# Kernel tuning notes

Measured on AMD Instinct MI355X. Metric: run time of the kernel, lower is better.

## Reference

```python
import jax, jax.numpy as jnp
import numpy as np

N_D, E_D = 50000, 200000
N_A, E_A = 50000, 200000
B, L, VOCAB = 256, 1000, 26


def _gat(x, src, dst, W, a_src, a_dst, bias, heads, dout, n,
         edge_attr=None, W_e=None, a_e=None):
    """PyG GATConv (eval mode: dropout off). Adds self-loops (default), edge-attr
    self-loops filled with mean (fill_value='mean' default), LeakyReLU(0.2),
    per-destination softmax, sum-aggregate, concat heads, add bias."""
    loop = jnp.arange(n, dtype=src.dtype)
    src = jnp.concatenate([src, loop])
    dst = jnp.concatenate([dst, loop])
    h = (x @ W).reshape(n, heads, dout)                      # [N,H,D]
    alpha = (h * a_src[None]).sum(-1)[src] + (h * a_dst[None]).sum(-1)[dst]  # [E',H]
    if edge_attr is not None:
        mean_e = jnp.mean(edge_attr, axis=0, keepdims=True)
        ea = jnp.concatenate([edge_attr, jnp.broadcast_to(mean_e, (n, edge_attr.shape[1]))], 0)
        he = (ea @ W_e).reshape(-1, heads, dout)             # [E',H,D]
        alpha = alpha + (he * a_e[None]).sum(-1)
    alpha = jax.nn.leaky_relu(alpha, 0.2)
    amax = jax.ops.segment_max(alpha, dst, num_segments=n)
    ex = jnp.exp(alpha - amax[dst])
    denom = jax.ops.segment_sum(ex, dst, num_segments=n)
    w = ex / (denom[dst] + 1e-16)                            # edge softmax weights
    out = jax.ops.segment_sum(h[src] * w[..., None], dst, num_segments=n)
    return out.reshape(n, heads * dout) + bias


def _conv1d(x, w):
    return jax.lax.conv_general_dilated(x, w, (1,), 'VALID',
                                        dimension_numbers=('NCH', 'OIH', 'NCH'))


def setup_inputs():
    key = jax.random.key(0)
    ks = iter(jax.random.split(key, 64))
    def nrm(shape, s=0.1):
        return jax.random.normal(next(ks), shape, jnp.float32) * s
    inp = {}
    inp['drug_x'] = nrm((N_D, 78), 1.0)
    inp['drug_edge_index'] = jax.random.randint(next(ks), (2, E_D), 0, N_D, jnp.int32)
    inp['drug_batch'] = ((jnp.arange(N_D) * B) // N_D).astype(jnp.int32)
    inp['target_tokens'] = jax.random.randint(next(ks), (B, L), 0, VOCAB, jnp.int32)
    inp['a2h_x'] = nrm((N_A, 24), 1.0)
    inp['a2h_edge_index'] = jax.random.randint(next(ks), (2, E_A), 0, N_A, jnp.int32)
    inp['a2h_edge_attr'] = nrm((E_A, 5), 1.0)
    inp['a2h_batch'] = ((jnp.arange(N_A) * B) // N_A).astype(jnp.int32)
    inp['gat1_w'] = nrm((78, 390)); inp['gat1_att_src'] = nrm((5, 78)); inp['gat1_att_dst'] = nrm((5, 78)); inp['gat1_bias'] = jnp.zeros((390,), jnp.float32)
    inp['gat2_w'] = nrm((390, 128)); inp['gat2_att_src'] = nrm((1, 128)); inp['gat2_att_dst'] = nrm((1, 128)); inp['gat2_bias'] = jnp.zeros((128,), jnp.float32)
    inp['fc_g1_w'] = nrm((128, 128)); inp['fc_g1_b'] = jnp.zeros((128,), jnp.float32)
    inp['embed_xt'] = nrm((VOCAB, 128), 1.0)
    inp['conv1_w'] = nrm((64, 128, 5)); inp['conv1_b'] = jnp.zeros((64,), jnp.float32)
    inp['conv2_w'] = nrm((32, 64, 3)); inp['conv2_b'] = jnp.zeros((32,), jnp.float32)
    inp['fc_xt1_w'] = nrm((32, 128)); inp['fc_xt1_b'] = jnp.zeros((128,), jnp.float32)
    inp['ag1_w'] = nrm((24, 320)); inp['ag1_att_src'] = nrm((5, 64)); inp['ag1_att_dst'] = nrm((5, 64)); inp['ag1_lin_edge'] = nrm((5, 320)); inp['ag1_att_edge'] = nrm((5, 64)); inp['ag1_bias'] = jnp.zeros((320,), jnp.float32)
    inp['ag2_w'] = nrm((320, 128)); inp['ag2_att_src'] = nrm((1, 128)); inp['ag2_att_dst'] = nrm((1, 128)); inp['ag2_lin_edge'] = nrm((5, 128)); inp['ag2_att_edge'] = nrm((1, 128)); inp['ag2_bias'] = jnp.zeros((128,), jnp.float32)
    inp['a2h_fc1_w'] = nrm((128, 128)); inp['a2h_fc1_b'] = jnp.zeros((128,), jnp.float32)
    inp['fc1_w'] = nrm((384, 1024)); inp['fc1_b'] = jnp.zeros((1024,), jnp.float32)
    inp['fc2_w'] = nrm((1024, 256)); inp['fc2_b'] = jnp.zeros((256,), jnp.float32)
    inp['out_w'] = nrm((256, 1)); inp['out_b'] = jnp.zeros((1,), jnp.float32)
    return inp


def reference(drug_x, drug_edge_index, drug_batch, target_tokens,
              a2h_x, a2h_edge_index, a2h_edge_attr, a2h_batch,
              gat1_w, gat1_att_src, gat1_att_dst, gat1_bias,
              gat2_w, gat2_att_src, gat2_att_dst, gat2_bias,
              fc_g1_w, fc_g1_b, embed_xt,
              conv1_w, conv1_b, conv2_w, conv2_b, fc_xt1_w, fc_xt1_b,
              ag1_w, ag1_att_src, ag1_att_dst, ag1_lin_edge, ag1_att_edge, ag1_bias,
              ag2_w, ag2_att_src, ag2_att_dst, ag2_lin_edge, ag2_att_edge, ag2_bias,
              a2h_fc1_w, a2h_fc1_b, fc1_w, fc1_b, fc2_w, fc2_b, out_w, out_b):
    # drug GAT branch (dropout is identity in eval mode)
    x = jax.nn.elu(_gat(drug_x, drug_edge_index[0], drug_edge_index[1],
                        gat1_w, gat1_att_src, gat1_att_dst, gat1_bias, 5, 78, N_D))
    x = jax.nn.relu(_gat(x, drug_edge_index[0], drug_edge_index[1],
                         gat2_w, gat2_att_src, gat2_att_dst, gat2_bias, 1, 128, N_D))
    x = jax.ops.segment_max(x, drug_batch, num_segments=B)        # global_max_pool
    x = jax.nn.relu(x @ fc_g1_w + fc_g1_b)
    # protein CNN branch
    e = embed_xt[target_tokens]                                   # [B,L,128]
    c = jnp.transpose(e, (0, 2, 1))                               # [B,128,L]
    c = jax.nn.relu(_conv1d(c, conv1_w) + conv1_b[None, :, None])
    c = jax.nn.relu(_conv1d(c, conv2_w) + conv2_b[None, :, None])
    xt = jnp.max(c, axis=-1) @ fc_xt1_w + fc_xt1_b                # AdaptiveMaxPool1d(1)
    # a2h GAT branch with edge features
    a = jax.nn.elu(_gat(a2h_x, a2h_edge_index[0], a2h_edge_index[1],
                        ag1_w, ag1_att_src, ag1_att_dst, ag1_bias, 5, 64, N_A,
                        a2h_edge_attr, ag1_lin_edge, ag1_att_edge))
    a = jax.nn.relu(_gat(a, a2h_edge_index[0], a2h_edge_index[1],
                         ag2_w, ag2_att_src, ag2_att_dst, ag2_bias, 1, 128, N_A,
                         a2h_edge_attr, ag2_lin_edge, ag2_att_edge))
    a = jax.ops.segment_max(a, a2h_batch, num_segments=B)
    a = jax.nn.relu(a @ a2h_fc1_w + a2h_fc1_b)
    # fusion head
    xc = jnp.concatenate([x, xt, a], axis=1)                      # [B,384]
    xc = jax.nn.relu(xc @ fc1_w + fc1_b)
    xc = jax.nn.relu(xc @ fc2_w + fc2_b)
    return xc @ out_w + out_b                                     # [B,1]
```

## Files before the change

kernel.cpp:

```cpp
#include <hip/hip_runtime.h>

#define NN 50000
#define EE 200000
#define BB 256
#define LL 1000

static inline int cdiv(int a, int b){ return (a + b - 1) / b; }

typedef __attribute__((ext_vector_type(4))) float f32x4;
typedef __attribute__((ext_vector_type(2))) float f32x2;
typedef __attribute__((ext_vector_type(8))) short bf16x8;

__device__ inline short f2bf(float f){
  unsigned u = __float_as_uint(f);
  unsigned r = u + 0x7fffu + ((u >> 16) & 1u);
  return (short)(r >> 16);
}
__device__ inline float bf2f(short s){
  return __uint_as_float(((unsigned)(unsigned short)s) << 16);
}

__global__ void zero_kernel(unsigned* __restrict__ p, long n){
  long i = (long)blockIdx.x*blockDim.x + threadIdx.x;
  long st = (long)gridDim.x*blockDim.x;
  for(; i < n; i += st) p[i] = 0u;
}

__global__ __launch_bounds__(256) void gemm_splitk_kernel(
    const float* __restrict__ A, const float* __restrict__ B,
    float* __restrict__ part, int M, int N, int K, int KS){
  __shared__ float As[32][17];
  const int tid = threadIdx.x;
  const int col = blockIdx.x*64 + (tid & 63);
  const int rg = tid >> 6;
  const int row0 = blockIdx.y*32;
  const int kc = (K + KS - 1) / KS;
  const int k0 = blockIdx.z * kc;
  const int k1 = min(k0 + kc, K);
  float acc[8] = {};
  for(int kb = k0; kb < k1; kb += 16){
    int kn = min(16, k1 - kb);
    for(int i = tid; i < 32*16; i += 256){
      int r = i >> 4, kk = i & 15;
      int gr = row0 + r;
      As[r][kk] = (gr < M && kb + kk < k1) ? A[(long)gr*K + kb + kk] : 0.f;
    }
    __syncthreads();
    if(col < N){
      for(int kk = 0; kk < kn; kk++){
        float b = B[(long)(kb+kk)*N + col];
        #pragma unroll
        for(int i = 0; i < 8; i++)
          acc[i] = fmaf(As[rg*8 + i][kk], b, acc[i]);
      }
    }
    __syncthreads();
  }
  if(col < N){
    #pragma unroll
    for(int i = 0; i < 8; i++){
      int r = row0 + rg*8 + i;
      if(r < M) part[((long)blockIdx.z*M + r)*N + col] = acc[i];
    }
  }
}

template<int ACT>
__global__ void splitk_reduce_kernel(const float* __restrict__ part,
                                     const float* __restrict__ bias,
                                     float* __restrict__ C,
                                     int M, int N, int KS, int ldc){
  int idx = blockIdx.x*256 + threadIdx.x;
  if(idx >= M*N) return;
  int r = idx / N, c = idx - r*N;
  float s = 0.f;
  for(int z = 0; z < KS; z++) s += part[((long)z*M + r)*N + c];
  s += bias[c];
  if(ACT == 1) s = fmaxf(s, 0.f);
  C[(long)r*ldc + c] = s;
}

__global__ __launch_bounds__(256) void gemm_mfma_bf16_kernel(
    const float* __restrict__ A, const float* __restrict__ B,
    short* __restrict__ C, int M, int N, int K, int ldc){
  __shared__ short As[128*32];
  __shared__ short Bs[64*32];
  const int tid = threadIdx.x;
  const int wave = tid >> 6, lane = tid & 63;
  const int wm = wave >> 1, wn = wave & 1;
  const int row0 = blockIdx.y*128, col0 = blockIdx.x*64;
  const int lrow = lane & 15;
  const int kslot = lane >> 4;
  const int bn = tid & 63, bs = tid >> 6;
  f32x4 acc[4][2] = {};
  for(int k0 = 0; k0 < K; k0 += 32){
    #pragma unroll
    for(int id = tid; id < 512; id += 256){
      int r = id >> 2, s = id & 3;
      int grow = row0 + r, gk = k0 + s*8;
      short vs[8];
      if(grow < M && gk + 7 < K){
        const float* p = A + (long)grow*K + gk;
        #pragma unroll
        for(int i = 0; i < 8; i += 2){
          f32x2 x = *(const f32x2*)(p + i);
          vs[i] = f2bf(x.x); vs[i+1] = f2bf(x.y);
        }
      } else {
        #pragma unroll
        for(int i = 0; i < 8; i++){
          float f = (grow < M && gk + i < K) ? A[(long)grow*K + gk + i] : 0.f;
          vs[i] = f2bf(f);
        }
      }
      *(bf16x8*)&As[r*32 + (s ^ ((r>>1)&3))*8] = *(const bf16x8*)vs;
    }
    {
      int gn = col0 + bn, gk = k0 + bs*8;
      short vs[8];
      #pragma unroll
      for(int i = 0; i < 8; i++){
        float f = (gn < N && gk + i < K) ? B[(long)(gk+i)*N + gn] : 0.f;
        vs[i] = f2bf(f);
      }
      *(bf16x8*)&Bs[bn*32 + (bs ^ ((bn>>1)&3))*8] = *(const bf16x8*)vs;
    }
    __syncthreads();
    bf16x8 af[4], bfr[2];
    #pragma unroll
    for(int mt = 0; mt < 4; mt++){
      int r = wm*64 + mt*16 + lrow;
      af[mt] = *(const bf16x8*)&As[r*32 + (kslot ^ ((r>>1)&3))*8];
    }
    #pragma unroll
    for(int nt = 0; nt < 2; nt++){
      int r = wn*32 + nt*16 + lrow;
      bfr[nt] = *(const bf16x8*)&Bs[r*32 + (kslot ^ ((r>>1)&3))*8];
    }
    #pragma unroll
    for(int mt = 0; mt < 4; mt++)
      #pragma unroll
      for(int nt = 0; nt < 2; nt++)
        acc[mt][nt] = __builtin_amdgcn_mfma_f32_16x16x32_bf16(af[mt], bfr[nt], acc[mt][nt], 0, 0, 0);
    __syncthreads();
  }
  #pragma unroll
  for(int mt = 0; mt < 4; mt++){
    #pragma unroll
    for(int nt = 0; nt < 2; nt++){
      #pragma unroll
      for(int rg = 0; rg < 4; rg++){
        int row = row0 + wm*64 + mt*16 + (lane>>4)*4 + rg;
        int col = col0 + wn*32 + nt*16 + (lane&15);
        if(row < M && col < N)
          C[(long)row*ldc + col] = f2bf(acc[mt][nt][rg]);
      }
    }
  }
}

__global__ __launch_bounds__(256) void gemm_mfma_bf16in_kernel(
    const short* __restrict__ A, int lda, const float* __restrict__ B,
    short* __restrict__ C, int M, int N, int K, int ldc){
  __shared__ short As[128*32];
  __shared__ short Bs[64*32];
  const int tid = threadIdx.x;
  const int wave = tid >> 6, lane = tid & 63;
  const int wm = wave >> 1, wn = wave & 1;
  const int row0 = blockIdx.y*128, col0 = blockIdx.x*64;
  const int lrow = lane & 15;
  const int kslot = lane >> 4;
  const int bn = tid & 63, bs = tid >> 6;
  f32x4 acc[4][2] = {};
  for(int k0 = 0; k0 < K; k0 += 32){
    #pragma unroll
    for(int id = tid; id < 512; id += 256){
      int r = id >> 2, s = id & 3;
      int grow = row0 + r, gk = k0 + s*8;
      short vs[8];
      if(grow < M && gk + 7 < K){
        *(bf16x8*)vs = *(const bf16x8*)&A[(long)grow*lda + gk];
      } else {
        #pragma unroll
        for(int i = 0; i < 8; i++)
          vs[i] = (grow < M && gk + i < K) ? A[(long)grow*lda + gk + i] : (short)0;
      }
      *(bf16x8*)&As[r*32 + (s ^ ((r>>1)&3))*8] = *(const bf16x8*)vs;
    }
    {
      int gn = col0 + bn, gk = k0 + bs*8;
      short vs[8];
      #pragma unroll
      for(int i = 0; i < 8; i++){
        float f = (gn < N && gk + i < K) ? B[(long)(gk+i)*N + gn] : 0.f;
        vs[i] = f2bf(f);
      }
      *(bf16x8*)&Bs[bn*32 + (bs ^ ((bn>>1)&3))*8] = *(const bf16x8*)vs;
    }
    __syncthreads();
    bf16x8 af[4], bfr[2];
    #pragma unroll
    for(int mt = 0; mt < 4; mt++){
      int r = wm*64 + mt*16 + lrow;
      af[mt] = *(const bf16x8*)&As[r*32 + (kslot ^ ((r>>1)&3))*8];
    }
    #pragma unroll
    for(int nt = 0; nt < 2; nt++){
      int r = wn*32 + nt*16 + lrow;
      bfr[nt] = *(const bf16x8*)&Bs[r*32 + (kslot ^ ((r>>1)&3))*8];
    }
    #pragma unroll
    for(int mt = 0; mt < 4; mt++)
      #pragma unroll
      for(int nt = 0; nt < 2; nt++)
        acc[mt][nt] = __builtin_amdgcn_mfma_f32_16x16x32_bf16(af[mt], bfr[nt], acc[mt][nt], 0, 0, 0);
    __syncthreads();
  }
  #pragma unroll
  for(int mt = 0; mt < 4; mt++){
    #pragma unroll
    for(int nt = 0; nt < 2; nt++){
      #pragma unroll
      for(int rg = 0; rg < 4; rg++){
        int row = row0 + wm*64 + mt*16 + (lane>>4)*4 + rg;
        int col = col0 + wn*32 + nt*16 + (lane&15);
        if(row < M && col < N)
          C[(long)row*ldc + col] = f2bf(acc[mt][nt][rg]);
      }
    }
  }
}

__global__ void wext_kernel(const float* __restrict__ W, const float* __restrict__ asrc,
                            const float* __restrict__ adst, float* __restrict__ WEXT,
                            int K, int F, int H, int D){
  int NE = F + 2*H;
  int t = blockIdx.x*blockDim.x + threadIdx.x;
  if(t >= K*NE) return;
  int k = t / NE, c = t - k*NE;
  float v;
  if(c < F){
    v = W[(long)k*F + c];
  } else {
    int cc = c - F;
    int h = cc >> 1;
    const float* a = (cc & 1) ? (adst + h*D) : (asrc + h*D);
    const float* wr = W + (long)k*F + h*D;
    float s = 0.f;
    for(int d = 0; d < D; d++) s = fmaf(wr[d], a[d], s);
    v = s;
  }
  WEXT[t] = v;
}

__global__ void extract_scores_kernel(const short* __restrict__ HB, float* __restrict__ SS,
                                      float* __restrict__ SD, int N, int H, int F, int ldh){
  int t = blockIdx.x*blockDim.x + threadIdx.x;
  if(t >= N*H) return;
  int n = t / H, hh = t - n*H;
  const short* p = HB + (long)n*ldh + F + 2*hh;
  SS[t] = bf2f(p[0]);
  SD[t] = bf2f(p[1]);
}

__global__ void count_kernel(const int* __restrict__ dst, int* __restrict__ deg, int E, int N){
  int e = blockIdx.x*blockDim.x + threadIdx.x;
  if(e >= E + N) return;
  int d = (e < E) ? dst[e] : (e - E);
  atomicAdd(&deg[d], 1);
}

__global__ void scan_sums_kernel(const int* __restrict__ deg, int* __restrict__ bsum, int n){
  __shared__ int red[256];
  int base = blockIdx.x*1024 + threadIdx.x*4;
  int s = 0;
  #pragma unroll
  for(int i = 0; i < 4; i++){ int idx = base + i; if(idx < n) s += deg[idx]; }
  red[threadIdx.x] = s;
  __syncthreads();
  for(int off = 128; off >= 1; off >>= 1){
    if((int)threadIdx.x < off) red[threadIdx.x] += red[threadIdx.x + off];
    __syncthreads();
  }
  if(threadIdx.x == 0) bsum[blockIdx.x] = red[0];
}

__global__ void scan_bsum_kernel(int* __restrict__ bsum, int nb){
  int lane = threadIdx.x;
  int v = (lane < nb) ? bsum[lane] : 0;
  for(int off = 1; off < 64; off <<= 1){
    int t = __shfl_up(v, off, 64);
    if(lane >= off) v += t;
  }
  int ex = __shfl_up(v, 1, 64);
  if(lane == 0) ex = 0;
  if(lane < nb) bsum[lane] = ex;
}

__global__ void scan_final_kernel(const int* __restrict__ deg, const int* __restrict__ bsum,
                                  int* __restrict__ indptr, int* __restrict__ cursor, int n){
  __shared__ int red[256];
  const int t = threadIdx.x;
  int base = blockIdx.x*1024 + t*4;
  int v[4]; int s = 0;
  #pragma unroll
  for(int i = 0; i < 4; i++){ int idx = base + i; v[i] = (idx < n) ? deg[idx] : 0; s += v[i]; }
  red[t] = s;
  __syncthreads();
  for(int off = 1; off < 256; off <<= 1){
    int val = (t >= off) ? red[t - off] : 0;
    __syncthreads();
    red[t] += val;
    __syncthreads();
  }
  int run = bsum[blockIdx.x] + ((t > 0) ? red[t-1] : 0);
  #pragma unroll
  for(int i = 0; i < 4; i++){
    int idx = base + i;
    if(idx < n){
      cursor[idx] = run;
      run += v[i];
      indptr[idx+1] = run;
    }
  }
  if(blockIdx.x == 0 && t == 0) indptr[0] = 0;
}

__global__ void scatter_kernel(const int* __restrict__ src, const int* __restrict__ dst,
                               int* __restrict__ cursor, int* __restrict__ ebuf,
                               int* __restrict__ srcp, int* __restrict__ dstp, int E, int N){
  int e = blockIdx.x*blockDim.x + threadIdx.x;
  if(e >= E + N) return;
  int d = (e < E) ? dst[e] : (e - E);
  int s = (e < E) ? src[e] : (e - E);
  int pos = atomicAdd(&cursor[d], 1);
  ebuf[pos] = e;
  srcp[pos] = s;
  dstp[pos] = d;
}

__global__ void meansum_part_kernel(const float* __restrict__ ea, float* __restrict__ partial, int E){
  __shared__ float red[256*5];
  float loc[5] = {0.f,0.f,0.f,0.f,0.f};
  for(int e = blockIdx.x*blockDim.x + threadIdx.x; e < E; e += gridDim.x*blockDim.x){
    #pragma unroll
    for(int k = 0; k < 5; k++) loc[k] += ea[(long)e*5 + k];
  }
  #pragma unroll
  for(int k = 0; k < 5; k++) red[threadIdx.x*5 + k] = loc[k];
  __syncthreads();
  for(int off = 128; off >= 1; off >>= 1){
    if((int)threadIdx.x < off){
      #pragma unroll
      for(int k = 0; k < 5; k++)
        red[threadIdx.x*5 + k] += red[(threadIdx.x + off)*5 + k];
    }
    __syncthreads();
  }
  if(threadIdx.x < 5) partial[blockIdx.x*5 + threadIdx.x] = red[threadIdx.x];
}

__global__ void meansum_final_kernel(const float* __restrict__ partial, float* __restrict__ sum5, int nb){
  int k = threadIdx.x;
  if(k >= 5) return;
  float s = 0.f;
  for(int b = 0; b < nb; b++) s += partial[b*5 + k];
  sum5[k] = s;
}

__global__ void edgeM_kernel(const float* __restrict__ We, const float* __restrict__ ae,
                             const float* __restrict__ sum5, float* __restrict__ Mout,
                             float* __restrict__ loopOut, int H, int D, float invE){
  __shared__ float Msh[25];
  int t = threadIdx.x;
  if(t < 5*H){
    int k = t / H, hh = t % H;
    float s = 0.f;
    for(int d = 0; d < D; d++) s = fmaf(We[(long)k*H*D + hh*D + d], ae[hh*D + d], s);
    Msh[t] = s;
    Mout[t] = s;
  }
  __syncthreads();
  if(t < H){
    float s = 0.f;
    for(int k = 0; k < 5; k++) s = fmaf(sum5[k]*invE, Msh[k*H + t], s);
    loopOut[t] = s;
  }
}

__global__ void alpha_csr_kernel(const int* __restrict__ ebuf, const int* __restrict__ srcp,
                                 const int* __restrict__ dstp,
                                 const float* __restrict__ ssrc, const float* __restrict__ sdst,
                                 const float* __restrict__ eattr, const float* __restrict__ M,
                                 const float* __restrict__ loopS, float* __restrict__ alpha,
                                 int E, int N, int H){
  int p = blockIdx.x*blockDim.x + threadIdx.x;
  if(p >= E + N) return;
  int e = ebuf[p], s = srcp[p], d = dstp[p];
  float ea[5];
  if(eattr && e < E){
    #pragma unroll
    for(int k = 0; k < 5; k++) ea[k] = eattr[(long)e*5 + k];
  }
  for(int hh = 0; hh < H; hh++){
    float a = ssrc[s*H + hh] + sdst[d*H + hh];
    if(eattr){
      if(e < E){
        float es = 0.f;
        #pragma unroll
        for(int k = 0; k < 5; k++) es = fmaf(ea[k], M[k*H + hh], es);
        a += es;
      } else {
        a += loopS[hh];
      }
    }
    a = a > 0.f ? a : 0.2f*a;
    alpha[(long)p*H + hh] = a;
  }
}

__global__ void statsweights_kernel(const int* __restrict__ indptr,
                                    const float* __restrict__ alpha,
                                    float* __restrict__ W, int N, int H){
  int t = blockIdx.x*blockDim.x + threadIdx.x;
  if(t >= N*H) return;
  int n = t / H, hh = t - n*H;
  int b0 = indptr[n], b1 = indptr[n+1];
  float m = -1e30f;
  for(int i = b0; i < b1; i++) m = fmaxf(m, alpha[(long)i*H + hh]);
  float s = 0.f;
  for(int i = b0; i < b1; i++) s += expf(alpha[(long)i*H + hh] - m);
  float inv = 1.f / (s + 1e-16f);
  for(int i = b0; i < b1; i++)
    W[(long)i*H + hh] = expf(alpha[(long)i*H + hh] - m) * inv;
}

template<int H, int D>
__global__ __launch_bounds__(256) void aggregate_kernel(
    const int* __restrict__ indptr, const int* __restrict__ srcp,
    const float* __restrict__ W, const short* __restrict__ hfeat,
    const float* __restrict__ bias, short* __restrict__ out,
    int ldh, int ldx, int act){
  constexpr int F = H*D;
  constexpr int CH = F/2;
  constexpr int NS = (CH + 63)/64;
  const int wave = threadIdx.x >> 6, lane = threadIdx.x & 63;
  const int n = blockIdx.x*4 + wave;
  if(n >= NN) return;
  const int b0 = indptr[n], b1 = indptr[n+1];
  f32x2 acc[NS];
  int hidx[NS];
  #pragma unroll
  for(int s = 0; s < NS; s++){
    acc[s].x = 0.f; acc[s].y = 0.f;
    int c = lane + 64*s;
    hidx[s] = (c < CH) ? (2*c)/D : 0;
  }
  int i = b0;
  for(; i + 1 < b1; i += 2){
    int sv0 = srcp[i], sv1 = srcp[i+1];
    const short* hr0 = hfeat + (long)sv0*ldh;
    const short* hr1 = hfeat + (long)sv1*ldh;
    #pragma unroll
    for(int s = 0; s < NS; s++){
      int c = lane + 64*s;
      if(c < CH){
        float w0 = W[(long)i*H + hidx[s]];
        float w1 = W[(long)(i+1)*H + hidx[s]];
        unsigned u0 = *(const unsigned*)&hr0[2*c];
        unsigned u1 = *(const unsigned*)&hr1[2*c];
        acc[s].x = fmaf(w0, __uint_as_float((u0 & 0xffffu) << 16), acc[s].x);
        acc[s].y = fmaf(w0, __uint_as_float(u0 & 0xffff0000u), acc[s].y);
        acc[s].x = fmaf(w1, __uint_as_float((u1 & 0xffffu) << 16), acc[s].x);
        acc[s].y = fmaf(w1, __uint_as_float(u1 & 0xffff0000u), acc[s].y);
      }
    }
  }
  if(i < b1){
    int sv = srcp[i];
    const short* hr = hfeat + (long)sv*ldh;
    #pragma unroll
    for(int s = 0; s < NS; s++){
      int c = lane + 64*s;
      if(c < CH){
        float w = W[(long)i*H + hidx[s]];
        unsigned u = *(const unsigned*)&hr[2*c];
        acc[s].x = fmaf(w, __uint_as_float((u & 0xffffu) << 16), acc[s].x);
        acc[s].y = fmaf(w, __uint_as_float(u & 0xffff0000u), acc[s].y);
      }
    }
  }
  #pragma unroll
  for(int s = 0; s < NS; s++){
    int c = lane + 64*s;
    if(c < CH){
      int f = 2*c;
      f32x2 b = *(const f32x2*)&bias[f];
      float v0 = acc[s].x + b.x;
      float v1 = acc[s].y + b.y;
      if(act == 1){ v0 = fmaxf(v0, 0.f); v1 = fmaxf(v1, 0.f); }
      else { v0 = v0 > 0.f ? v0 : expm1f(v0); v1 = v1 > 0.f ? v1 : expm1f(v1); }
      unsigned pu = ((unsigned)(unsigned short)f2bf(v0)) |
                    (((unsigned)(unsigned short)f2bf(v1)) << 16);
      *(unsigned*)&out[(long)n*ldx + f] = pu;
    }
  }
}

__global__ __launch_bounds__(256) void pool_batch_kernel(
    const short* __restrict__ x, float* __restrict__ out){
  const int b = blockIdx.x;
  const int F = 128;
  int n0 = (int)(((long)b*NN + BB - 1) / BB);
  int n1 = (int)(((long)(b+1)*NN + BB - 1) / BB);
  if(n1 > NN) n1 = NN;
  const int f = threadIdx.x & (F-1);
  const int half = threadIdx.x >> 7;
  float m = -1e30f;
  for(int n = n0 + half; n < n1; n += 2)
    m = fmaxf(m, bf2f(x[(long)n*F + f]));
  __shared__ float red[256];
  red[threadIdx.x] = m;
  __syncthreads();
  if(half == 0)
    out[b*F + f] = fmaxf(red[threadIdx.x], red[threadIdx.x + 128]);
}

__global__ void embw_kernel(const float* __restrict__ emb, const float* __restrict__ w1,
                            float* __restrict__ embW){
  int t = blockIdx.x*blockDim.x + threadIdx.x;
  if(t >= 26*5*64) return;
  int oc = t & 63;
  int kk = (t >> 6) % 5;
  int v = t / (5*64);
  float s = 0.f;
  for(int ic = 0; ic < 128; ic++) s = fmaf(emb[v*128 + ic], w1[(oc*128 + ic)*5 + kk], s);
  embW[(v*5 + kk)*64 + oc] = s;
}

#define C1_TP 128
__global__ void conv1_kernel(const int* __restrict__ tokens, const float* __restrict__ embW,
                             const float* __restrict__ b1, short* __restrict__ c1){
  __shared__ float T[26*5*64];
  __shared__ int tok[C1_TP + 4];
  int b = blockIdx.y;
  int p0 = blockIdx.x * C1_TP;
  for(int i = threadIdx.x; i < 2080; i += 256)
    *(f32x4*)&T[i*4] = *(const f32x4*)&embW[i*4];
  int ntok = min(C1_TP + 4, LL - p0);
  for(int i = threadIdx.x; i < ntok; i += 256) tok[i] = tokens[b*LL + p0 + i];
  __syncthreads();
  int oc = threadIdx.x & 63;
  int ps = threadIdx.x >> 6;
  float bias = b1[oc];
  int np = min(C1_TP, 996 - p0);
  for(int pp = ps; pp < np; pp += 4){
    float acc = bias;
    #pragma unroll
    for(int kk = 0; kk < 5; kk++) acc += T[(tok[pp+kk]*5 + kk)*64 + oc];
    c1[((long)b*996 + p0 + pp)*64 + oc] = f2bf(fmaxf(acc, 0.f));
  }
}

__global__ __launch_bounds__(256) void conv2_mfma_kernel(
    const short* __restrict__ c1, const float* __restrict__ w2,
    const float* __restrict__ b2, unsigned* __restrict__ xt_pre){
  __shared__ short X[66*64];
  __shared__ short Bs[6*32*32];
  const int tid = threadIdx.x;
  const int b = blockIdx.y;
  const int p0 = blockIdx.x*64;
  for(int t = tid; t < 6144; t += 256){
    int ks = t >> 10, rem = t & 1023;
    int n = rem >> 5, kl = rem & 31;
    int k = ks*32 + kl;
    int kk = k >> 6, ic = k & 63;
    Bs[ks*1024 + n*32 + (((kl>>3) ^ ((n>>1)&3))<<3) + (kl&7)] = f2bf(w2[(n*64 + ic)*3 + kk]);
  }
  for(int c = tid; c < 528; c += 256){
    int r = c >> 3, s = c & 7;
    short vs[8] = {0,0,0,0,0,0,0,0};
    if(p0 + r < 996)
      *(bf16x8*)vs = *(const bf16x8*)&c1[((long)b*996 + p0 + r)*64 + s*8];
    *(bf16x8*)&X[r*64 + ((s ^ (r&7))<<3)] = *(const bf16x8*)vs;
  }
  __syncthreads();
  const int w = tid >> 6, lane = tid & 63;
  const int lrow = lane & 15, kslot = lane >> 4;
  f32x4 acc[2] = {};
  #pragma unroll
  for(int ks = 0; ks < 6; ks++){
    int kk = ks >> 1;
    int r = w*16 + lrow + kk;
    int s = ((ks&1)*4 + kslot) ^ (r & 7);
    bf16x8 a = *(const bf16x8*)&X[r*64 + (s<<3)];
    #pragma unroll
    for(int nt = 0; nt < 2; nt++){
      int n = nt*16 + lrow;
      bf16x8 bfr = *(const bf16x8*)&Bs[ks*1024 + n*32 + ((kslot ^ ((n>>1)&3))<<3)];
      acc[nt] = __builtin_amdgcn_mfma_f32_16x16x32_bf16(a, bfr, acc[nt], 0, 0, 0);
    }
  }
  #pragma unroll
  for(int nt = 0; nt < 2; nt++){
    int oc = nt*16 + lrow;
    float bias = b2[oc];
    float m = 0.f;
    #pragma unroll
    for(int rg = 0; rg < 4; rg++){
      int prow = p0 + w*16 + kslot*4 + rg;
      float v = acc[nt][rg] + bias;
      if(prow < 994) m = fmaxf(m, v);
    }
    m = fmaxf(m, __shfl_xor(m, 16, 64));
    m = fmaxf(m, __shfl_xor(m, 32, 64));
    if(kslot == 0)
      atomicMax(&xt_pre[b*32 + oc], __float_as_uint(m));
  }
}

__global__ void head_final_kernel(const float* __restrict__ y2, const float* __restrict__ ow,
                                  const float* __restrict__ ob, float* __restrict__ out){
  int b = blockIdx.x*blockDim.x + threadIdx.x;
  if(b >= BB) return;
  float s = ob[0];
  for(int k = 0; k < 256; k++) s = fmaf(y2[b*256 + k], ow[k], s);
  out[b] = s;
}

extern "C" void kernel_launch(void* const* d_in, const int* in_sizes, int n_in,
                              void* d_out, int out_size, void* d_ws, size_t ws_size,
                              hipStream_t stream){
  const float* drug_x    = (const float*)d_in[0];
  const int*   drug_ei   = (const int*)  d_in[1];
  const int*   drug_b    = (const int*)  d_in[2];
  const int*   tokens    = (const int*)  d_in[3];
  const float* a2h_x     = (const float*)d_in[4];
  const int*   a2h_ei    = (const int*)  d_in[5];
  const float* a2h_ea    = (const float*)d_in[6];
  const int*   a2h_b     = (const int*)  d_in[7];
  const float* gat1_w    = (const float*)d_in[8];
  const float* gat1_as   = (const float*)d_in[9];
  const float* gat1_ad   = (const float*)d_in[10];
  const float* gat1_bias = (const float*)d_in[11];
  const float* gat2_w    = (const float*)d_in[12];
  const float* gat2_as   = (const float*)d_in[13];
  const float* gat2_ad   = (const float*)d_in[14];
  const float* gat2_bias = (const float*)d_in[15];
  const float* fc_g1_w   = (const float*)d_in[16];
  const float* fc_g1_b   = (const float*)d_in[17];
  const float* embed_xt  = (const float*)d_in[18];
  const float* conv1_w   = (const float*)d_in[19];
  const float* conv1_b   = (const float*)d_in[20];
  const float* conv2_w   = (const float*)d_in[21];
  const float* conv2_b   = (const float*)d_in[22];
  const float* fc_xt1_w  = (const float*)d_in[23];
  const float* fc_xt1_b  = (const float*)d_in[24];
  const float* ag1_w     = (const float*)d_in[25];
  const float* ag1_as    = (const float*)d_in[26];
  const float* ag1_ad    = (const float*)d_in[27];
  const float* ag1_le    = (const float*)d_in[28];
  const float* ag1_ae    = (const float*)d_in[29];
  const float* ag1_bias  = (const float*)d_in[30];
  const float* ag2_w     = (const float*)d_in[31];
  const float* ag2_as    = (const float*)d_in[32];
  const float* ag2_ad    = (const float*)d_in[33];
  const float* ag2_le    = (const float*)d_in[34];
  const float* ag2_ae    = (const float*)d_in[35];
  const float* ag2_bias  = (const float*)d_in[36];
  const float* afc1_w    = (const float*)d_in[37];
  const float* afc1_b    = (const float*)d_in[38];
  const float* fc1_w     = (const float*)d_in[39];
  const float* fc1_b     = (const float*)d_in[40];
  const float* fc2_w     = (const float*)d_in[41];
  const float* fc2_b     = (const float*)d_in[42];
  const float* out_w     = (const float*)d_in[43];
  const float* out_b     = (const float*)d_in[44];
  (void)drug_b; (void)a2h_b;

  char* ws = (char*)d_ws;
  size_t off = 0;
  auto alloc = [&](size_t bytes) -> void* {
    void* p = ws + off;
    off = (off + bytes + 255) & ~(size_t)255;
    return p;
  };
  short* HB     = (short*)alloc((size_t)NN*400*2);
  short* X1     = (short*)alloc((size_t)NN*392*2);
  float* SS     = (float*)alloc((size_t)NN*5*4);
  float* SD     = (float*)alloc((size_t)NN*5*4);
  float* ALPHA  = (float*)alloc((size_t)(EE+NN)*5*4);
  float* WBUF   = (float*)alloc((size_t)(EE+NN)*5*4);
  int*   INDPTR = (int*)alloc((size_t)(NN+1)*4);
  int*   DEGA   = (int*)alloc((size_t)NN*4);
  int*   CURSOR = (int*)alloc((size_t)NN*4);
  int*   BSUM   = (int*)alloc((size_t)64*4);
  int*   EBUF   = (int*)alloc((size_t)(EE+NN)*4);
  int*   SRCP   = (int*)alloc((size_t)(EE+NN)*4);
  int*   DSTP   = (int*)alloc((size_t)(EE+NN)*4);
  float* WEXT   = (float*)alloc((size_t)390*400*4);
  float* SUMP   = (float*)alloc((size_t)256*5*4);
  float* SUM5   = (float*)alloc(64);
  float* M1     = (float*)alloc(128);
  float* LOOP1  = (float*)alloc(64);
  float* M2     = (float*)alloc(64);
  float* LOOP2  = (float*)alloc(64);
  float* EMBW   = (float*)alloc((size_t)26*5*64*4);
  unsigned* XT_PRE = (unsigned*)alloc((size_t)BB*32*4);
  float* POOLG  = (float*)alloc((size_t)BB*128*4);
  float* POOLA  = (float*)alloc((size_t)BB*128*4);
  float* XC     = (float*)alloc((size_t)BB*384*4);
  float* Y1     = (float*)alloc((size_t)BB*1024*4);
  float* Y2     = (float*)alloc((size_t)BB*256*4);
  float* PART   = (float*)alloc((size_t)8*BB*1024*4);
  (void)ws_size; (void)in_sizes; (void)n_in; (void)out_size;

  int gEN = cdiv(EE + NN, 256);
  const int NB = cdiv(NN, 1024);

  auto build_csr = [&](const int* src, const int* dst){
    zero_kernel<<<cdiv(NN,256), 256, 0, stream>>>((unsigned*)DEGA, NN);
    count_kernel<<<gEN, 256, 0, stream>>>(dst, DEGA, EE, NN);
    scan_sums_kernel<<<NB, 256, 0, stream>>>(DEGA, BSUM, NN);
    scan_bsum_kernel<<<1, 64, 0, stream>>>(BSUM, NB);
    scan_final_kernel<<<NB, 256, 0, stream>>>(DEGA, BSUM, INDPTR, CURSOR, NN);
    scatter_kernel<<<gEN, 256, 0, stream>>>(src, dst, CURSOR, EBUF, SRCP, DSTP, EE, NN);
  };

  auto run_gat = [&](const void* xin, bool xbf16, int lda, int Kin,
                     const float* W, const float* asrc, const float* adst,
                     const float* bias, int H, int D, int act,
                     const float* eattr, const float* Mmat, const float* loopS,
                     short* xout, int ldx){
    int F = H*D;
    int NE = F + 2*H;
    int ldh = (NE + 7) & ~7;
    wext_kernel<<<cdiv(Kin*NE,256), 256, 0, stream>>>(W, asrc, adst, WEXT, Kin, F, H, D);
    dim3 g(cdiv(NE,64), cdiv(NN,128));
    if(xbf16)
      gemm_mfma_bf16in_kernel<<<g, 256, 0, stream>>>((const short*)xin, lda, WEXT, HB, NN, NE, Kin, ldh);
    else
      gemm_mfma_bf16_kernel<<<g, 256, 0, stream>>>((const float*)xin, WEXT, HB, NN, NE, Kin, ldh);
    extract_scores_kernel<<<cdiv(NN*H,256), 256, 0, stream>>>(HB, SS, SD, NN, H, F, ldh);
    alpha_csr_kernel<<<gEN, 256, 0, stream>>>(EBUF, SRCP, DSTP, SS, SD, eattr, Mmat, loopS,
                                              ALPHA, EE, NN, H);
    statsweights_kernel<<<cdiv(NN*H,256), 256, 0, stream>>>(INDPTR, ALPHA, WBUF, NN, H);
    dim3 ga(cdiv(NN,4));
    if(H == 5 && D == 78)
      aggregate_kernel<5,78><<<ga, 256, 0, stream>>>(INDPTR, SRCP, WBUF, HB, bias, xout, ldh, ldx, act);
    else if(H == 5 && D == 64)
      aggregate_kernel<5,64><<<ga, 256, 0, stream>>>(INDPTR, SRCP, WBUF, HB, bias, xout, ldh, ldx, act);
    else
      aggregate_kernel<1,128><<<ga, 256, 0, stream>>>(INDPTR, SRCP, WBUF, HB, bias, xout, ldh, ldx, act);
  };

  auto run_fc = [&](const float* A, const float* Bw, const float* bias, float* C,
                    int M, int N, int K, int KS, int act, int ldc){
    dim3 g(cdiv(N,64), cdiv(M,32), KS);
    gemm_splitk_kernel<<<g, 256, 0, stream>>>(A, Bw, PART, M, N, K, KS);
    int nout = M*N;
    if(act == 1)
      splitk_reduce_kernel<1><<<cdiv(nout,256), 256, 0, stream>>>(PART, bias, C, M, N, KS, ldc);
    else
      splitk_reduce_kernel<0><<<cdiv(nout,256), 256, 0, stream>>>(PART, bias, C, M, N, KS, ldc);
  };

  build_csr(drug_ei, drug_ei + EE);
  run_gat(drug_x, false, 0, 78, gat1_w, gat1_as, gat1_ad, gat1_bias, 5, 78, 2,
          nullptr, nullptr, nullptr, X1, 392);
  run_gat(X1, true, 392, 390, gat2_w, gat2_as, gat2_ad, gat2_bias, 1, 128, 1,
          nullptr, nullptr, nullptr, X1, 128);
  pool_batch_kernel<<<BB, 256, 0, stream>>>(X1, POOLG);
  run_fc(POOLG, fc_g1_w, fc_g1_b, XC + 0, BB, 128, 128, 1, 1, 384);

  build_csr(a2h_ei, a2h_ei + EE);
  meansum_part_kernel<<<256, 256, 0, stream>>>(a2h_ea, SUMP, EE);
  meansum_final_kernel<<<1, 64, 0, stream>>>(SUMP, SUM5, 256);
  edgeM_kernel<<<1, 64, 0, stream>>>(ag1_le, ag1_ae, SUM5, M1, LOOP1, 5, 64, 1.f/EE);
  edgeM_kernel<<<1, 64, 0, stream>>>(ag2_le, ag2_ae, SUM5, M2, LOOP2, 1, 128, 1.f/EE);
  run_gat(a2h_x, false, 0, 24, ag1_w, ag1_as, ag1_ad, ag1_bias, 5, 64, 2,
          a2h_ea, M1, LOOP1, X1, 320);
  run_gat(X1, true, 320, 320, ag2_w, ag2_as, ag2_ad, ag2_bias, 1, 128, 1,
          a2h_ea, M2, LOOP2, X1, 128);
  pool_batch_kernel<<<BB, 256, 0, stream>>>(X1, POOLA);
  run_fc(POOLA, afc1_w, afc1_b, XC + 256, BB, 128, 128, 1, 1, 384);

  embw_kernel<<<cdiv(26*5*64,256), 256, 0, stream>>>(embed_xt, conv1_w, EMBW);
  short* C1 = HB;
  conv1_kernel<<<dim3(cdiv(996, C1_TP), BB), 256, 0, stream>>>(tokens, EMBW, conv1_b, C1);
  zero_kernel<<<cdiv(BB*32,256), 256, 0, stream>>>(XT_PRE, (long)BB*32);
  conv2_mfma_kernel<<<dim3(16, BB), 256, 0, stream>>>(C1, conv2_w, conv2_b, XT_PRE);
  run_fc((const float*)XT_PRE, fc_xt1_w, fc_xt1_b, XC + 128, BB, 128, 32, 1, 0, 384);

  run_fc(XC, fc1_w, fc1_b, Y1, BB, 1024, 384, 3, 1, 1024);
  run_fc(Y1, fc2_w, fc2_b, Y2, BB, 256, 1024, 8, 1, 256);
  head_final_kernel<<<1, 256, 0, stream>>>(Y2, out_w, out_b, (float*)d_out);
}
```

Baseline: 778.8 us.

## Fuse edge alpha computation into softmax weights kernel, drop DSTP, unroll aggregation

Merges the per-edge alpha kernel into the per-destination softmax kernel, so attention logits are recomputed on the fly from source/destination scores and edge attributes instead of going through a materialized ALPHA buffer. The kernel now writes unnormalized exp weights and then rescales them, and the DSTP array and its scatter writes are removed. The aggregation loop is unrolled to four neighbors per step, and FC layers with no K split use a direct GEMM with fused bias and activation instead of split-K plus a reduce. The cost is that logits are computed twice per edge with gathers spread over each thread's CSR range, so memory traffic is less coalesced.

```diff
diff --git a/kernel.cpp b/kernel.cpp
--- a/kernel.cpp
+++ b/kernel.cpp
@@ -24,6 +24,49 @@
   long i = (long)blockIdx.x*blockDim.x + threadIdx.x;
   long st = (long)gridDim.x*blockDim.x;
   for(; i < n; i += st) p[i] = 0u;
+}
+
+template<int ACT>
+__global__ __launch_bounds__(256) void gemm_small_kernel(
+    const float* __restrict__ A, const float* __restrict__ B,
+    const float* __restrict__ bias, float* __restrict__ C,
+    int M, int N, int K, int ldc){
+  __shared__ float As[32][17];
+  const int tid = threadIdx.x;
+  const int col = blockIdx.x*64 + (tid & 63);
+  const int rg = tid >> 6;
+  const int row0 = blockIdx.y*32;
+  float acc[8] = {};
+  for(int kb = 0; kb < K; kb += 16){
+    int kn = min(16, K - kb);
+    for(int i = tid; i < 32*16; i += 256){
+      int r = i >> 4, kk = i & 15;
+      int gr = row0 + r;
+      As[r][kk] = (gr < M && kb + kk < K) ? A[(long)gr*K + kb + kk] : 0.f;
+    }
+    __syncthreads();
+    if(col < N){
+      for(int kk = 0; kk < kn; kk++){
+        float b = B[(long)(kb+kk)*N + col];
+        #pragma unroll
+        for(int i = 0; i < 8; i++)
+          acc[i] = fmaf(As[rg*8 + i][kk], b, acc[i]);
+      }
+    }
+    __syncthreads();
+  }
+  if(col < N){
+    float bs = bias[col];
+    #pragma unroll
+    for(int i = 0; i < 8; i++){
+      int r = row0 + rg*8 + i;
+      if(r < M){
+        float v = acc[i] + bs;
+        if(ACT == 1) v = fmaxf(v, 0.f);
+        C[(long)r*ldc + col] = v;
+      }
+    }
+  }
 }
 
 __global__ __launch_bounds__(256) void gemm_splitk_kernel(
@@ -328,7 +371,7 @@
 
 __global__ void scatter_kernel(const int* __restrict__ src, const int* __restrict__ dst,
                                int* __restrict__ cursor, int* __restrict__ ebuf,
-                               int* __restrict__ srcp, int* __restrict__ dstp, int E, int N){
+                               int* __restrict__ srcp, int E, int N){
   int e = blockIdx.x*blockDim.x + threadIdx.x;
   if(e >= E + N) return;
   int d = (e < E) ? dst[e] : (e - E);
@@ -336,7 +379,6 @@
   int pos = atomicAdd(&cursor[d], 1);
   ebuf[pos] = e;
   srcp[pos] = s;
-  dstp[pos] = d;
 }
 
 __global__ void meansum_part_kernel(const float* __restrict__ ea, float* __restrict__ partial, int E){
@@ -388,51 +430,52 @@
   }
 }
 
-__global__ void alpha_csr_kernel(const int* __restrict__ ebuf, const int* __restrict__ srcp,
-                                 const int* __restrict__ dstp,
-                                 const float* __restrict__ ssrc, const float* __restrict__ sdst,
-                                 const float* __restrict__ eattr, const float* __restrict__ M,
-                                 const float* __restrict__ loopS, float* __restrict__ alpha,
-                                 int E, int N, int H){
-  int p = blockIdx.x*blockDim.x + threadIdx.x;
-  if(p >= E + N) return;
-  int e = ebuf[p], s = srcp[p], d = dstp[p];
-  float ea[5];
-  if(eattr && e < E){
-    #pragma unroll
-    for(int k = 0; k < 5; k++) ea[k] = eattr[(long)e*5 + k];
-  }
-  for(int hh = 0; hh < H; hh++){
-    float a = ssrc[s*H + hh] + sdst[d*H + hh];
-    if(eattr){
-      if(e < E){
-        float es = 0.f;
-        #pragma unroll
-        for(int k = 0; k < 5; k++) es = fmaf(ea[k], M[k*H + hh], es);
-        a += es;
-      } else {
-        a += loopS[hh];
-      }
-    }
-    a = a > 0.f ? a : 0.2f*a;
-    alpha[(long)p*H + hh] = a;
-  }
-}
-
-__global__ void statsweights_kernel(const int* __restrict__ indptr,
-                                    const float* __restrict__ alpha,
-                                    float* __restrict__ W, int N, int H){
+__global__ void alpha_weights_kernel(const int* __restrict__ indptr, const int* __restrict__ ebuf,
+                                     const int* __restrict__ srcp,
+                                     const float* __restrict__ ssrc, const float* __restrict__ sdst,
+                                     const float* __restrict__ eattr, const float* __restrict__ M,
+                                     const float* __restrict__ loopS, float* __restrict__ W,
+                                     int E, int N, int H){
   int t = blockIdx.x*blockDim.x + threadIdx.x;
   if(t >= N*H) return;
   int n = t / H, hh = t - n*H;
   int b0 = indptr[n], b1 = indptr[n+1];
+  float sd = sdst[n*H + hh];
   float m = -1e30f;
-  for(int i = b0; i < b1; i++) m = fmaxf(m, alpha[(long)i*H + hh]);
-  float s = 0.f;
-  for(int i = b0; i < b1; i++) s += expf(alpha[(long)i*H + hh] - m);
-  float inv = 1.f / (s + 1e-16f);
+  for(int i = b0; i < b1; i++){
+    float a = ssrc[srcp[i]*H + hh] + sd;
+    if(eattr){
+      int e = ebuf[i];
+      if(e < E){
+        float es = 0.f;
+        #pragma unroll
+        for(int k = 0; k < 5; k++) es = fmaf(eattr[(long)e*5 + k], M[k*H + hh], es);
+        a += es;
+      } else a += loopS[hh];
+    }
+    a = a > 0.f ? a : 0.2f*a;
+    m = fmaxf(m, a);
+  }
+  float ssum = 0.f;
+  for(int i = b0; i < b1; i++){
+    float a = ssrc[srcp[i]*H + hh] + sd;
+    if(eattr){
+      int e = ebuf[i];
+      if(e < E){
+        float es = 0.f;
+        #pragma unroll
+        for(int k = 0; k < 5; k++) es = fmaf(eattr[(long)e*5 + k], M[k*H + hh], es);
+        a += es;
+      } else a += loopS[hh];
+    }
+    a = a > 0.f ? a : 0.2f*a;
+    float w = expf(a - m);
+    ssum += w;
+    W[(long)i*H + hh] = w;
+  }
+  float inv = 1.f / (ssum + 1e-16f);
   for(int i = b0; i < b1; i++)
-    W[(long)i*H + hh] = expf(alpha[(long)i*H + hh] - m) * inv;
+    W[(long)i*H + hh] *= inv;
 }
 
 template<int H, int D>
@@ -457,26 +500,36 @@
     hidx[s] = (c < CH) ? (2*c)/D : 0;
   }
   int i = b0;
-  for(; i + 1 < b1; i += 2){
-    int sv0 = srcp[i], sv1 = srcp[i+1];
-    const short* hr0 = hfeat + (long)sv0*ldh;
-    const short* hr1 = hfeat + (long)sv1*ldh;
+  for(; i + 3 < b1; i += 4){
+    int sv0 = srcp[i], sv1 = srcp[i+1], sv2 = srcp[i+2], sv3 = srcp[i+3];
+    const short* h0 = hfeat + (long)sv0*ldh;
+    const short* h1 = hfeat + (long)sv1*ldh;
+    const short* h2 = hfeat + (long)sv2*ldh;
+    const short* h3 = hfeat + (long)sv3*ldh;
     #pragma unroll
     for(int s = 0; s < NS; s++){
       int c = lane + 64*s;
       if(c < CH){
         float w0 = W[(long)i*H + hidx[s]];
         float w1 = W[(long)(i+1)*H + hidx[s]];
-        unsigned u0 = *(const unsigned*)&hr0[2*c];
-        unsigned u1 = *(const unsigned*)&hr1[2*c];
+        float w2 = W[(long)(i+2)*H + hidx[s]];
+        float w3 = W[(long)(i+3)*H + hidx[s]];
+        unsigned u0 = *(const unsigned*)&h0[2*c];
+        unsigned u1 = *(const unsigned*)&h1[2*c];
+        unsigned u2 = *(const unsigned*)&h2[2*c];
+        unsigned u3 = *(const unsigned*)&h3[2*c];
         acc[s].x = fmaf(w0, __uint_as_float((u0 & 0xffffu) << 16), acc[s].x);
         acc[s].y = fmaf(w0, __uint_as_float(u0 & 0xffff0000u), acc[s].y);
         acc[s].x = fmaf(w1, __uint_as_float((u1 & 0xffffu) << 16), acc[s].x);
         acc[s].y = fmaf(w1, __uint_as_float(u1 & 0xffff0000u), acc[s].y);
-      }
-    }
-  }
-  if(i < b1){
+        acc[s].x = fmaf(w2, __uint_as_float((u2 & 0xffffu) << 16), acc[s].x);
+        acc[s].y = fmaf(w2, __uint_as_float(u2 & 0xffff0000u), acc[s].y);
+        acc[s].x = fmaf(w3, __uint_as_float((u3 & 0xffffu) << 16), acc[s].x);
+        acc[s].y = fmaf(w3, __uint_as_float(u3 & 0xffff0000u), acc[s].y);
+      }
+    }
+  }
+  for(; i < b1; i++){
     int sv = srcp[i];
     const short* hr = hfeat + (long)sv*ldh;
     #pragma unroll
@@ -689,7 +742,6 @@
   short* X1     = (short*)alloc((size_t)NN*392*2);
   float* SS     = (float*)alloc((size_t)NN*5*4);
   float* SD     = (float*)alloc((size_t)NN*5*4);
-  float* ALPHA  = (float*)alloc((size_t)(EE+NN)*5*4);
   float* WBUF   = (float*)alloc((size_t)(EE+NN)*5*4);
   int*   INDPTR = (int*)alloc((size_t)(NN+1)*4);
   int*   DEGA   = (int*)alloc((size_t)NN*4);
@@ -697,7 +749,6 @@
   int*   BSUM   = (int*)alloc((size_t)64*4);
   int*   EBUF   = (int*)alloc((size_t)(EE+NN)*4);
   int*   SRCP   = (int*)alloc((size_t)(EE+NN)*4);
-  int*   DSTP   = (int*)alloc((size_t)(EE+NN)*4);
   float* WEXT   = (float*)alloc((size_t)390*400*4);
   float* SUMP   = (float*)alloc((size_t)256*5*4);
   float* SUM5   = (float*)alloc(64);
@@ -724,7 +775,7 @@
     scan_sums_kernel<<<NB, 256, 0, stream>>>(DEGA, BSUM, NN);
     scan_bsum_kernel<<<1, 64, 0, stream>>>(BSUM, NB);
     scan_final_kernel<<<NB, 256, 0, stream>>>(DEGA, BSUM, INDPTR, CURSOR, NN);
-    scatter_kernel<<<gEN, 256, 0, stream>>>(src, dst, CURSOR, EBUF, SRCP, DSTP, EE, NN);
+    scatter_kernel<<<gEN, 256, 0, stream>>>(src, dst, CURSOR, EBUF, SRCP, EE, NN);
   };
 
   auto run_gat = [&](const void* xin, bool xbf16, int lda, int Kin,
@@ -742,9 +793,8 @@
     else
       gemm_mfma_bf16_kernel<<<g, 256, 0, stream>>>((const float*)xin, WEXT, HB, NN, NE, Kin, ldh);
     extract_scores_kernel<<<cdiv(NN*H,256), 256, 0, stream>>>(HB, SS, SD, NN, H, F, ldh);
-    alpha_csr_kernel<<<gEN, 256, 0, stream>>>(EBUF, SRCP, DSTP, SS, SD, eattr, Mmat, loopS,
-                                              ALPHA, EE, NN, H);
-    statsweights_kernel<<<cdiv(NN*H,256), 256, 0, stream>>>(INDPTR, ALPHA, WBUF, NN, H);
+    alpha_weights_kernel<<<cdiv(NN*H,256), 256, 0, stream>>>(INDPTR, EBUF, SRCP, SS, SD,
+                                                             eattr, Mmat, loopS, WBUF, EE, NN, H);
     dim3 ga(cdiv(NN,4));
     if(H == 5 && D == 78)
       aggregate_kernel<5,78><<<ga, 256, 0, stream>>>(INDPTR, SRCP, WBUF, HB, bias, xout, ldh, ldx, act);
@@ -756,6 +806,14 @@
 
   auto run_fc = [&](const float* A, const float* Bw, const float* bias, float* C,
                     int M, int N, int K, int KS, int act, int ldc){
+    if(KS == 1){
+      dim3 g(cdiv(N,64), cdiv(M,32));
+      if(act == 1)
+        gemm_small_kernel<1><<<g, 256, 0, stream>>>(A, Bw, bias, C, M, N, K, ldc);
+      else
+        gemm_small_kernel<0><<<g, 256, 0, stream>>>(A, Bw, bias, C, M, N, K, ldc);
+      return;
+    }
     dim3 g(cdiv(N,64), cdiv(M,32), KS);
     gemm_splitk_kernel<<<g, 256, 0, stream>>>(A, Bw, PART, M, N, K, KS);
     int nout = M*N;
```

Result: slower. 826.2 us (+6.1%).
